# Kernel optimization log

Measured on AMD Instinct MI355X. Metric: run time of the kernel, lower is better.

The kernel has to match this reference:

```python
import jax, jax.numpy as jnp
import numpy as np
from jax import lax

VOCAB, ENC_DIM, PRED_H, JOINT_H = 4096, 1024, 640, 640
T, MAX_SYM, BLANK, SOS = 128, 30, 0, -1
S = T * (MAX_SYM + 1)  # upper bound on greedy-decode loop iterations


def setup_inputs() -> dict:
    key = jax.random.key(0)
    ks = jax.random.split(key, 10)
    rn = lambda k, shape, s: jax.random.normal(k, shape, jnp.float32) * s
    return {
        "enc_out": rn(ks[0], (1, T, ENC_DIM), 1.0),
        "out_len": T,
        "emb": rn(ks[1], (VOCAB, PRED_H), 0.1),
        "Wih0": rn(ks[2], (4 * PRED_H, PRED_H), 0.04),
        "Whh0": rn(ks[3], (4 * PRED_H, PRED_H), 0.04),
        "b0": jnp.zeros((4 * PRED_H,), jnp.float32),
        "Wih1": rn(ks[4], (4 * PRED_H, PRED_H), 0.04),
        "Whh1": rn(ks[5], (4 * PRED_H, PRED_H), 0.04),
        "b1": jnp.zeros((4 * PRED_H,), jnp.float32),
        "Wj1": rn(ks[6], (JOINT_H, ENC_DIM + PRED_H), 0.03),
        "bj1": jnp.zeros((JOINT_H,), jnp.float32),
        "Wj2": rn(ks[7], (VOCAB, JOINT_H), 0.04),
        "bj2": jnp.zeros((VOCAB,), jnp.float32),
    }


def _lstm_cell(x, h, c, Wih, Whh, b):
    z = x @ Wih.T + h @ Whh.T + b  # [4H], torch gate order i,f,g,o
    i, f, g, o = jnp.split(z, 4)
    c2 = jax.nn.sigmoid(f) * c + jax.nn.sigmoid(i) * jnp.tanh(g)
    return jax.nn.sigmoid(o) * jnp.tanh(c2), c2


def _decode(enc_out, timesteps, emb, Wih0, Whh0, b0, Wih1, Whh1, b1, Wj1, bj1, Wj2, bj2):
    enc = enc_out[0]  # [T, ENC_DIM]

    def step(carry, _):
        t, sa, last, h0, c0, h1, c1, labels, cnt, done = carry
        # prediction net step (SOS = -1 -> zero embedding)
        g_in = jnp.where(last < 0, 0.0, emb[jnp.maximum(last, 0)])
        h0n, c0n = _lstm_cell(g_in, h0, c0, Wih0, Whh0, b0)
        h1n, c1n = _lstm_cell(h0n, h1, c1, Wih1, Whh1, b1)
        # joint net on current encoder frame
        f = enc[jnp.minimum(t, T - 1)]
        hid = jax.nn.relu(Wj1 @ jnp.concatenate([f, h1n]) + bj1)
        logits = Wj2 @ hid + bj2  # [VOCAB]
        k = jnp.argmax(logits).astype(jnp.int32)
        stop_sym = (k == BLANK) | (sa >= MAX_SYM)
        emit = (~stop_sym) & (~done)
        adv = stop_sym & (~done)
        # emit: append symbol, keep hidden'; blank/max: advance time, discard hidden'
        last2 = jnp.where(emit, k, last)
        h0 = jnp.where(emit, h0n, h0); c0 = jnp.where(emit, c0n, c0)
        h1 = jnp.where(emit, h1n, h1); c1 = jnp.where(emit, c1n, c1)
        labels = labels.at[cnt].set(jnp.where(emit, k, labels[cnt]))
        cnt2 = cnt + emit.astype(jnp.int32)
        sa2 = jnp.where(emit, sa + 1, jnp.where(adv, 0, sa))
        t2 = t + adv.astype(jnp.int32)
        done2 = done | (adv & (t2 >= timesteps))
        out_logits = jnp.where(done, 0.0, logits)
        return (t2, sa2, last2, h0, c0, h1, c1, labels, cnt2, done2), out_logits

    zeros = jnp.zeros((PRED_H,), jnp.float32)
    carry0 = (jnp.int32(0), jnp.int32(0), jnp.int32(SOS),
              zeros, zeros, zeros, zeros,
              jnp.full((S,), -1, jnp.int32), jnp.int32(0), jnp.bool_(False))
    carry, logits_seq = lax.scan(step, carry0, None, length=S)
    labels, cnt = carry[7], carry[8]
    return logits_seq, labels, cnt


def reference(enc_out, out_len, emb, Wih0, Whh0, b0, Wih1, Whh1, b1, Wj1, bj1, Wj2, bj2):
    return _decode(enc_out, out_len, emb, Wih0, Whh0, b0, Wih1, Whh1, b1, Wj1, bj1, Wj2, bj2)
```

## Files before the change

kernel.cpp:

```cpp
#include <hip/hip_runtime.h>
#include <cmath>

#define VOCAB   4096
#define ENC_DIM 1024
#define PRED_H  640
#define JOINT_H 640
#define TMAX    128
#define MAX_SYM 30
#define NSTEPS  (TMAX*(MAX_SYM+1))
#define NWG     256
#define NTHR    512
#define RLX __ATOMIC_RELAXED
#define AGT __HIP_MEMORY_SCOPE_AGENT

typedef unsigned long long u64;


__device__ __forceinline__ float wave_red(float v){
  v += __shfl_xor(v, 32, 64);
  v += __shfl_xor(v, 16, 64);
  v += __shfl_xor(v,  8, 64);
  v += __shfl_xor(v,  4, 64);
  v += __shfl_xor(v,  2, 64);
  v += __shfl_xor(v,  1, 64);
  return v;
}

__device__ __forceinline__ float sigf(float x){ return 1.0f/(1.0f+expf(-x)); }

__device__ __forceinline__ void tstore(u64* p, float v, unsigned tag){
  __hip_atomic_store(p, ((u64)tag<<32) | (u64)__float_as_uint(v), RLX, AGT);
}
__device__ __forceinline__ float tpollv(u64* p, unsigned tag){
  u64 e = __hip_atomic_load(p, RLX, AGT);
  while ((unsigned)(e>>32) != tag){
    __builtin_amdgcn_s_sleep(4);
    e = __hip_atomic_load(p, RLX, AGT);
  }
  return __uint_as_float((unsigned)e);
}

__device__ __forceinline__ u64 mkentry(float lg, int r, unsigned ep){
  unsigned u = __float_as_uint(lg);
  u = (u & 0x80000000u) ? ~u : (u | 0x80000000u);
  return ((u64)u<<24) | ((u64)(ep&0xFFFu)<<12) | (u64)(4095 - r);
}

__global__ void init_ws(unsigned* ws){
  for (int i = threadIdx.x; i < 8192; i += 256) ws[i] = 0u;
}

__global__ __launch_bounds__(NTHR, 2)
void rnnt_decode(const float* __restrict__ enc,
                 const int*   __restrict__ outlen_p,
                 const float* __restrict__ emb,
                 const float* __restrict__ Wih0, const float* __restrict__ Whh0, const float* __restrict__ b0,
                 const float* __restrict__ Wih1, const float* __restrict__ Whh1, const float* __restrict__ b1,
                 const float* __restrict__ Wj1,  const float* __restrict__ bj1,
                 const float* __restrict__ Wj2,  const float* __restrict__ bj2,
                 float* __restrict__ out,
                 u64* __restrict__ parts,
                 u64* __restrict__ bufsT,
                 u64* __restrict__ hidT)
{
  const int wg = blockIdx.x, tid = threadIdx.x;
  const int wave = tid >> 6, lane = tid & 63;
  const int timesteps = outlen_p[0];

  __shared__ float xa[PRED_H];
  __shared__ float xsh[ENC_DIM];
  __shared__ float h0buf[2][PRED_H];
  __shared__ float h1buf[2][PRED_H];
  __shared__ float hidsh[JOINT_H];
  __shared__ float zsh[4][4];
  __shared__ float zjs[8];
  __shared__ float c0c[4], c1c[4], c0p[4], c1p[4];
  __shared__ u64 psh[8];
  __shared__ u64 pmx[4];

  const int jb = (wg*PRED_H)/NWG;
  const int je = ((wg+1)*PRED_H)/NWG;
  const int nj = je - jb;

  const int riA = wave, riB = wave + 8;
  const int gA = riA & 3, jA = riA >> 2;
  const int gB = riB & 3, jBx = riB >> 2;
  const bool hasB = (riB < 4*nj);
  const int rowA = gA*PRED_H + jb + jA;
  const int rowB = hasB ? (gB*PRED_H + jb + jBx) : 0;

  float w0xA[10], w0hA[10], w0xB[10], w0hB[10];
  float w1xA[10], w1hA[10], w1xB[10], w1hB[10];
  #pragma unroll
  for (int i = 0; i < 10; ++i){
    int c = lane + (i<<6);
    w0xA[i] = Wih0[(size_t)rowA*PRED_H + c];
    w0hA[i] = Whh0[(size_t)rowA*PRED_H + c];
    w1xA[i] = Wih1[(size_t)rowA*PRED_H + c];
    w1hA[i] = Whh1[(size_t)rowA*PRED_H + c];
    w0xB[i] = hasB ? Wih0[(size_t)rowB*PRED_H + c] : 0.f;
    w0hB[i] = hasB ? Whh0[(size_t)rowB*PRED_H + c] : 0.f;
    w1xB[i] = hasB ? Wih1[(size_t)rowB*PRED_H + c] : 0.f;
    w1hB[i] = hasB ? Whh1[(size_t)rowB*PRED_H + c] : 0.f;
  }
  const float bA0 = b0[rowA], bA1 = b1[rowA];
  const float bB0 = hasB ? b0[rowB] : 0.f, bB1 = hasB ? b1[rowB] : 0.f;

  const int vt = (wave < 4) ? wave*64 + lane : (wave-4)*64 + lane;
  float wjf0[4], wjh0[3], wjf2[4], wjh2[3];
  {
    int r0 = (wave < 4) ? jb : jb + 1;
    #pragma unroll
    for (int i = 0; i < 4; ++i) wjf0[i] = Wj1[(size_t)r0*(ENC_DIM+PRED_H) + vt + (i<<8)];
    #pragma unroll
    for (int i = 0; i < 3; ++i){
      int c = vt + (i<<8);
      wjh0[i] = (c < PRED_H) ? Wj1[(size_t)r0*(ENC_DIM+PRED_H) + ENC_DIM + c] : 0.f;
    }
    #pragma unroll
    for (int i = 0; i < 4; ++i) wjf2[i] = 0.f;
    #pragma unroll
    for (int i = 0; i < 3; ++i) wjh2[i] = 0.f;
    if (wave < 4 && nj == 3){
      int r2 = jb + 2;
      #pragma unroll
      for (int i = 0; i < 4; ++i) wjf2[i] = Wj1[(size_t)r2*(ENC_DIM+PRED_H) + vt + (i<<8)];
      #pragma unroll
      for (int i = 0; i < 3; ++i){
        int c = vt + (i<<8);
        wjh2[i] = (c < PRED_H) ? Wj1[(size_t)r2*(ENC_DIM+PRED_H) + ENC_DIM + c] : 0.f;
      }
    }
  }
  float bjr[3];
  bjr[0] = bj1[jb]; bjr[1] = bj1[jb+1]; bjr[2] = (nj == 3) ? bj1[jb+2] : 0.f;
  float ca0 = 0.f, ca2 = 0.f;

  const int rA2 = wg*16 + wave*2, rB2 = rA2 + 1;
  float wj2A[10], wj2B[10];
  #pragma unroll
  for (int i = 0; i < 10; ++i){
    int c = lane + (i<<6);
    wj2A[i] = Wj2[(size_t)rA2*JOINT_H + c];
    wj2B[i] = Wj2[(size_t)rB2*JOINT_H + c];
  }
  const float bjA2 = bj2[rA2], bjB2 = bj2[rB2];

  for (int i = tid; i < PRED_H; i += NTHR){ h0buf[0][i] = 0.f; h1buf[0][i] = 0.f; }
  if (tid < 4){ c0c[tid] = 0.f; c1c[tid] = 0.f; }
  __syncthreads();

  int cur = 0, t = 0, sa = 0, last = -1, cnt = 0, tStaged = -1;
  bool done = false, reuse = false;

  for (int s = 0; s < NSTEPS; ++s){
    if (done){
      if (wg < 8) out[(size_t)s*VOCAB + wg*NTHR + tid] = 0.f;
      continue;
    }
    const unsigned tag = (unsigned)(s + 1);

    if (!reuse){
      for (int i = tid; i < PRED_H; i += NTHR)
        xa[i] = (last >= 0) ? emb[(size_t)last*PRED_H + i] : 0.f;
      __syncthreads();
      {
        float acc = 0.f;
        #pragma unroll
        for (int i = 0; i < 10; ++i) acc = fmaf(w0xA[i], xa[lane+(i<<6)], acc);
        #pragma unroll
        for (int i = 0; i < 10; ++i) acc = fmaf(w0hA[i], h0buf[cur][lane+(i<<6)], acc);
        acc = wave_red(acc);
        if (lane == 0) zsh[gA][jA] = acc + bA0;
        if (hasB){
          float a2 = 0.f;
          #pragma unroll
          for (int i = 0; i < 10; ++i) a2 = fmaf(w0xB[i], xa[lane+(i<<6)], a2);
          #pragma unroll
          for (int i = 0; i < 10; ++i) a2 = fmaf(w0hB[i], h0buf[cur][lane+(i<<6)], a2);
          a2 = wave_red(a2);
          if (lane == 0) zsh[gB][jBx] = a2 + bB0;
        }
      }
      __syncthreads();
      if (tid < nj){
        float ig = sigf(zsh[0][tid]), fg = sigf(zsh[1][tid]);
        float gg = tanhf(zsh[2][tid]), og = sigf(zsh[3][tid]);
        float c2 = fg*c0c[tid] + ig*gg;
        c0p[tid] = c2;
        tstore(&bufsT[jb+tid], og*tanhf(c2), tag);
      }
      __syncthreads();

      for (int i = tid; i < PRED_H; i += NTHR)
        h0buf[cur^1][i] = tpollv(&bufsT[i], tag);
      __syncthreads();
      {
        float acc = 0.f;
        #pragma unroll
        for (int i = 0; i < 10; ++i) acc = fmaf(w1xA[i], h0buf[cur^1][lane+(i<<6)], acc);
        #pragma unroll
        for (int i = 0; i < 10; ++i) acc = fmaf(w1hA[i], h1buf[cur][lane+(i<<6)], acc);
        acc = wave_red(acc);
        if (lane == 0) zsh[gA][jA] = acc + bA1;
        if (hasB){
          float a2 = 0.f;
          #pragma unroll
          for (int i = 0; i < 10; ++i) a2 = fmaf(w1xB[i], h0buf[cur^1][lane+(i<<6)], a2);
          #pragma unroll
          for (int i = 0; i < 10; ++i) a2 = fmaf(w1hB[i], h1buf[cur][lane+(i<<6)], a2);
          a2 = wave_red(a2);
          if (lane == 0) zsh[gB][jBx] = a2 + bB1;
        }
      }
      __syncthreads();
      if (tid < nj){
        float ig = sigf(zsh[0][tid]), fg = sigf(zsh[1][tid]);
        float gg = tanhf(zsh[2][tid]), og = sigf(zsh[3][tid]);
        float c2 = fg*c1c[tid] + ig*gg;
        c1p[tid] = c2;
        tstore(&bufsT[PRED_H+jb+tid], og*tanhf(c2), tag);
      }
    }

    {
      int tcap = (t < TMAX-1) ? t : (TMAX-1);
      bool fNew = (tcap != tStaged);
      if (fNew)
        for (int i = tid; i < ENC_DIM; i += NTHR) xsh[i] = enc[(size_t)tcap*ENC_DIM + i];
      if (!reuse)
        for (int i = tid; i < PRED_H; i += NTHR)
          h1buf[cur^1][i] = tpollv(&bufsT[PRED_H+i], tag);
      __syncthreads();
      if (fNew){
        float a = 0.f;
        #pragma unroll
        for (int i = 0; i < 4; ++i) a = fmaf(wjf0[i], xsh[vt+(i<<8)], a);
        ca0 = a;
        if (wave < 4 && nj == 3){
          float a2 = 0.f;
          #pragma unroll
          for (int i = 0; i < 4; ++i) a2 = fmaf(wjf2[i], xsh[vt+(i<<8)], a2);
          ca2 = a2;
        }
        tStaged = tcap;
      }
      {
        float acc = ca0;
        #pragma unroll
        for (int i = 0; i < 3; ++i){
          int c = vt + (i<<8);
          acc = fmaf(wjh0[i], h1buf[cur^1][(c < PRED_H) ? c : 0], acc);
        }
        acc = wave_red(acc);
        if (lane == 0) zjs[wave] = acc;
      }
      __syncthreads();
      if (tid == 0){
        float v0 = zjs[0]+zjs[1]+zjs[2]+zjs[3] + bjr[0];
        tstore(&hidT[jb],   v0 > 0.f ? v0 : 0.f, tag);
        float v1 = zjs[4]+zjs[5]+zjs[6]+zjs[7] + bjr[1];
        tstore(&hidT[jb+1], v1 > 0.f ? v1 : 0.f, tag);
      }
      if (nj == 3){
        __syncthreads();
        if (wave < 4){
          float acc = ca2;
          #pragma unroll
          for (int i = 0; i < 3; ++i){
            int c = vt + (i<<8);
            acc = fmaf(wjh2[i], h1buf[cur^1][(c < PRED_H) ? c : 0], acc);
          }
          acc = wave_red(acc);
          if (lane == 0) zjs[wave] = acc;
        }
        __syncthreads();
        if (tid == 0){
          float v2 = zjs[0]+zjs[1]+zjs[2]+zjs[3] + bjr[2];
          tstore(&hidT[jb+2], v2 > 0.f ? v2 : 0.f, tag);
        }
      }
    }

    int k;
    {
      for (int i = tid; i < JOINT_H; i += NTHR)
        hidsh[i] = tpollv(&hidT[i], tag);
      __syncthreads();
      float accA = 0.f, accB = 0.f;
      #pragma unroll
      for (int i = 0; i < 10; ++i){
        float h = hidsh[lane+(i<<6)];
        accA = fmaf(wj2A[i], h, accA);
        accB = fmaf(wj2B[i], h, accB);
      }
      accA = wave_red(accA);
      accB = wave_red(accB);
      if (lane == 0){
        float lgA = accA + bjA2, lgB = accB + bjB2;
        out[(size_t)s*VOCAB + rA2] = lgA;
        out[(size_t)s*VOCAB + rB2] = lgB;
        u64 eA = mkentry(lgA, rA2, tag), eB = mkentry(lgB, rB2, tag);
        psh[wave] = eA > eB ? eA : eB;
      }
      __syncthreads();
      if (tid == 0){
        u64 m = psh[0];
        #pragma unroll
        for (int w = 1; w < 8; ++w) if (psh[w] > m) m = psh[w];
        __hip_atomic_store(&parts[wg], m, RLX, AGT);
      }
      u64 myp = 0;
      if (tid < 256){
        u64 e = __hip_atomic_load(&parts[tid], RLX, AGT);
        while ((unsigned)((e>>12) & 0xFFFu) != (tag & 0xFFFu)){
          __builtin_amdgcn_s_sleep(2);
          e = __hip_atomic_load(&parts[tid], RLX, AGT);
        }
        myp = e;
      }
      if (wave < 4){
        #pragma unroll
        for (int off = 32; off; off >>= 1){
          u64 o = __shfl_xor(myp, off, 64);
          if (o > myp) myp = o;
        }
        if (lane == 0) pmx[wave] = myp;
      }
      __syncthreads();
      u64 m = pmx[0];
      if (pmx[1] > m) m = pmx[1];
      if (pmx[2] > m) m = pmx[2];
      if (pmx[3] > m) m = pmx[3];
      k = 4095 - (int)(m & 0xFFFull);
    }

    bool stop = (k == 0) || (sa >= MAX_SYM);
    if (!stop){
      if (wg == 0 && tid == 0) out[(size_t)NSTEPS*VOCAB + cnt] = (float)k;
      if (tid < nj){ c0c[tid] = c0p[tid]; c1c[tid] = c1p[tid]; }
      cnt++; sa++; last = k; cur ^= 1; reuse = false;
    } else {
      sa = 0; t++; reuse = true;
      if (t >= timesteps) done = true;
    }
    __syncthreads();
  }

  size_t lab = (size_t)NSTEPS*VOCAB;
  int gidx = wg*NTHR + tid;
  for (int i = cnt + gidx; i < NSTEPS; i += NWG*NTHR) out[lab + i] = -1.f;
  if (wg == 0 && tid == 0) out[lab + NSTEPS] = (float)cnt;
}

extern "C" void kernel_launch(void* const* d_in, const int* in_sizes, int n_in,
                              void* d_out, int out_size, void* d_ws, size_t ws_size,
                              hipStream_t stream) {
  const float* enc  = (const float*)d_in[0];
  const int*   olen = (const int*)  d_in[1];
  const float* emb  = (const float*)d_in[2];
  const float* Wih0 = (const float*)d_in[3];
  const float* Whh0 = (const float*)d_in[4];
  const float* b0   = (const float*)d_in[5];
  const float* Wih1 = (const float*)d_in[6];
  const float* Whh1 = (const float*)d_in[7];
  const float* b1   = (const float*)d_in[8];
  const float* Wj1  = (const float*)d_in[9];
  const float* bj1  = (const float*)d_in[10];
  const float* Wj2  = (const float*)d_in[11];
  const float* bj2  = (const float*)d_in[12];
  float* out = (float*)d_out;

  u64* parts = (u64*)d_ws;
  u64* bufsT = (u64*)((char*)d_ws + 4096);
  u64* hidT  = (u64*)((char*)d_ws + 16384);

  init_ws<<<1, 256, 0, stream>>>((unsigned*)d_ws);

  void* args[] = {&enc,&olen,&emb,&Wih0,&Whh0,&b0,&Wih1,&Whh1,&b1,
                  &Wj1,&bj1,&Wj2,&bj2,&out,&parts,&bufsT,&hidT};
  hipLaunchCooperativeKernel((const void*)rnnt_decode, dim3(NWG), dim3(NTHR),
                             args, 0, stream);
}
```

Baseline: 51.19 ms.

## Replace tagged per-element polling with counter barriers and vector cache-bypass loads

Swaps the per-element tagged 64-bit stores and polls for plain float stores plus a per-phase atomic arrival counter. One thread per workgroup spins on the counter, then 160 threads fetch the shared vector with dwordx4 loads that bypass the cache. The argmax partials drop the epoch tag and use the same counter, and the third joint-hidden row is computed alongside the first two, which removes extra syncthreads. The aim is fewer global atomics and polls on each step of the serial decode, at the cost of relying on release ordering through waitcnt before the relaxed counter increment.

```diff
diff --git a/kernel.cpp b/kernel.cpp
--- a/kernel.cpp
+++ b/kernel.cpp
@@ -14,6 +14,8 @@
 #define AGT __HIP_MEMORY_SCOPE_AGENT
 
 typedef unsigned long long u64;
+typedef __attribute__((ext_vector_type(4))) float f32x4;
+typedef __attribute__((ext_vector_type(4))) unsigned int u32x4;
 
 
 __device__ __forceinline__ float wave_red(float v){
@@ -28,22 +30,28 @@
 
 __device__ __forceinline__ float sigf(float x){ return 1.0f/(1.0f+expf(-x)); }
 
-__device__ __forceinline__ void tstore(u64* p, float v, unsigned tag){
-  __hip_atomic_store(p, ((u64)tag<<32) | (u64)__float_as_uint(v), RLX, AGT);
-}
-__device__ __forceinline__ float tpollv(u64* p, unsigned tag){
-  u64 e = __hip_atomic_load(p, RLX, AGT);
-  while ((unsigned)(e>>32) != tag){
-    __builtin_amdgcn_s_sleep(4);
-    e = __hip_atomic_load(p, RLX, AGT);
-  }
-  return __uint_as_float((unsigned)e);
-}
-
-__device__ __forceinline__ u64 mkentry(float lg, int r, unsigned ep){
+__device__ __forceinline__ void cstore_f(float* p, float v){
+  __hip_atomic_store((unsigned*)p, __float_as_uint(v), RLX, AGT);
+}
+__device__ __forceinline__ void cstore_u64(u64* p, u64 v){
+  __hip_atomic_store(p, v, RLX, AGT);
+}
+
+__device__ __forceinline__ f32x4 cload_f4(const float* p){
+  f32x4 r;
+  asm volatile("global_load_dwordx4 %0, %1, off sc0 sc1" : "=v"(r) : "v"(p));
+  return r;
+}
+__device__ __forceinline__ u32x4 cload_u4(const u64* p){
+  u32x4 r;
+  asm volatile("global_load_dwordx4 %0, %1, off sc0 sc1" : "=v"(r) : "v"(p));
+  return r;
+}
+
+__device__ __forceinline__ u64 mkentry(float lg, int r){
   unsigned u = __float_as_uint(lg);
   u = (u & 0x80000000u) ? ~u : (u | 0x80000000u);
-  return ((u64)u<<24) | ((u64)(ep&0xFFFu)<<12) | (u64)(4095 - r);
+  return ((u64)u<<32) | (u64)(4095 - r);
 }
 
 __global__ void init_ws(unsigned* ws){
@@ -59,13 +67,17 @@
                  const float* __restrict__ Wj1,  const float* __restrict__ bj1,
                  const float* __restrict__ Wj2,  const float* __restrict__ bj2,
                  float* __restrict__ out,
+                 unsigned* __restrict__ cnts,
                  u64* __restrict__ parts,
-                 u64* __restrict__ bufsT,
-                 u64* __restrict__ hidT)
+                 float* __restrict__ h0n,
+                 float* __restrict__ h1n,
+                 float* __restrict__ hidg)
 {
   const int wg = blockIdx.x, tid = threadIdx.x;
   const int wave = tid >> 6, lane = tid & 63;
   const int timesteps = outlen_p[0];
+  unsigned* cntA = cnts;      unsigned* cntB = cnts + 16;
+  unsigned* cntH = cnts + 32; unsigned* cntP = cnts + 48;
 
   __shared__ float xa[PRED_H];
   __shared__ float xsh[ENC_DIM];
@@ -74,9 +86,11 @@
   __shared__ float hidsh[JOINT_H];
   __shared__ float zsh[4][4];
   __shared__ float zjs[8];
+  __shared__ float zjs2[4];
   __shared__ float c0c[4], c1c[4], c0p[4], c1p[4];
   __shared__ u64 psh[8];
-  __shared__ u64 pmx[4];
+  __shared__ u64 pm[128];
+  __shared__ int kshm;
 
   const int jb = (wg*PRED_H)/NWG;
   const int je = ((wg+1)*PRED_H)/NWG;
@@ -151,6 +165,7 @@
   __syncthreads();
 
   int cur = 0, t = 0, sa = 0, last = -1, cnt = 0, tStaged = -1;
+  unsigned eA = 0, eB = 0, eH = 0, eP = 0;
   bool done = false, reuse = false;
 
   for (int s = 0; s < NSTEPS; ++s){
@@ -158,9 +173,9 @@
       if (wg < 8) out[(size_t)s*VOCAB + wg*NTHR + tid] = 0.f;
       continue;
     }
-    const unsigned tag = (unsigned)(s + 1);
 
     if (!reuse){
+      ++eA; ++eB;
       for (int i = tid; i < PRED_H; i += NTHR)
         xa[i] = (last >= 0) ? emb[(size_t)last*PRED_H + i] : 0.f;
       __syncthreads();
@@ -188,12 +203,22 @@
         float gg = tanhf(zsh[2][tid]), og = sigf(zsh[3][tid]);
         float c2 = fg*c0c[tid] + ig*gg;
         c0p[tid] = c2;
-        tstore(&bufsT[jb+tid], og*tanhf(c2), tag);
-      }
-      __syncthreads();
-
-      for (int i = tid; i < PRED_H; i += NTHR)
-        h0buf[cur^1][i] = tpollv(&bufsT[i], tag);
+        cstore_f(&h0n[jb+tid], og*tanhf(c2));
+      }
+      asm volatile("s_waitcnt vmcnt(0)" ::: "memory");
+      if (tid == 0) __hip_atomic_fetch_add(cntA, 1u, RLX, AGT);
+
+      if (tid == 0){
+        while (__hip_atomic_load(cntA, RLX, AGT) < eA*NWG) __builtin_amdgcn_s_sleep(1);
+      }
+      __syncthreads();
+      {
+        f32x4 v;
+        if (tid < 160) v = cload_f4(h0n + (tid<<2));
+        asm volatile("s_waitcnt vmcnt(0)" ::: "memory");
+        __builtin_amdgcn_sched_barrier(0);
+        if (tid < 160) *(f32x4*)&h0buf[cur^1][tid<<2] = v;
+      }
       __syncthreads();
       {
         float acc = 0.f;
@@ -219,18 +244,29 @@
         float gg = tanhf(zsh[2][tid]), og = sigf(zsh[3][tid]);
         float c2 = fg*c1c[tid] + ig*gg;
         c1p[tid] = c2;
-        tstore(&bufsT[PRED_H+jb+tid], og*tanhf(c2), tag);
-      }
+        cstore_f(&h1n[jb+tid], og*tanhf(c2));
+      }
+      asm volatile("s_waitcnt vmcnt(0)" ::: "memory");
+      if (tid == 0) __hip_atomic_fetch_add(cntB, 1u, RLX, AGT);
     }
 
     {
+      ++eH;
       int tcap = (t < TMAX-1) ? t : (TMAX-1);
       bool fNew = (tcap != tStaged);
       if (fNew)
         for (int i = tid; i < ENC_DIM; i += NTHR) xsh[i] = enc[(size_t)tcap*ENC_DIM + i];
-      if (!reuse)
-        for (int i = tid; i < PRED_H; i += NTHR)
-          h1buf[cur^1][i] = tpollv(&bufsT[PRED_H+i], tag);
+      if (!reuse){
+        if (tid == 0){
+          while (__hip_atomic_load(cntB, RLX, AGT) < eB*NWG) __builtin_amdgcn_s_sleep(1);
+        }
+        __syncthreads();
+        f32x4 v;
+        if (tid < 160) v = cload_f4(h1n + (tid<<2));
+        asm volatile("s_waitcnt vmcnt(0)" ::: "memory");
+        __builtin_amdgcn_sched_barrier(0);
+        if (tid < 160) *(f32x4*)&h1buf[cur^1][tid<<2] = v;
+      }
       __syncthreads();
       if (fNew){
         float a = 0.f;
@@ -255,37 +291,45 @@
         acc = wave_red(acc);
         if (lane == 0) zjs[wave] = acc;
       }
+      if (wave < 4 && nj == 3){
+        float acc = ca2;
+        #pragma unroll
+        for (int i = 0; i < 3; ++i){
+          int c = vt + (i<<8);
+          acc = fmaf(wjh2[i], h1buf[cur^1][(c < PRED_H) ? c : 0], acc);
+        }
+        acc = wave_red(acc);
+        if (lane == 0) zjs2[wave] = acc;
+      }
       __syncthreads();
       if (tid == 0){
         float v0 = zjs[0]+zjs[1]+zjs[2]+zjs[3] + bjr[0];
-        tstore(&hidT[jb],   v0 > 0.f ? v0 : 0.f, tag);
+        cstore_f(&hidg[jb],   v0 > 0.f ? v0 : 0.f);
         float v1 = zjs[4]+zjs[5]+zjs[6]+zjs[7] + bjr[1];
-        tstore(&hidT[jb+1], v1 > 0.f ? v1 : 0.f, tag);
-      }
-      if (nj == 3){
-        __syncthreads();
-        if (wave < 4){
-          float acc = ca2;
-          #pragma unroll
-          for (int i = 0; i < 3; ++i){
-            int c = vt + (i<<8);
-            acc = fmaf(wjh2[i], h1buf[cur^1][(c < PRED_H) ? c : 0], acc);
-          }
-          acc = wave_red(acc);
-          if (lane == 0) zjs[wave] = acc;
-        }
-        __syncthreads();
-        if (tid == 0){
-          float v2 = zjs[0]+zjs[1]+zjs[2]+zjs[3] + bjr[2];
-          tstore(&hidT[jb+2], v2 > 0.f ? v2 : 0.f, tag);
-        }
+        cstore_f(&hidg[jb+1], v1 > 0.f ? v1 : 0.f);
+        if (nj == 3){
+          float v2 = zjs2[0]+zjs2[1]+zjs2[2]+zjs2[3] + bjr[2];
+          cstore_f(&hidg[jb+2], v2 > 0.f ? v2 : 0.f);
+        }
+        asm volatile("s_waitcnt vmcnt(0)" ::: "memory");
+        __hip_atomic_fetch_add(cntH, 1u, RLX, AGT);
       }
     }
 
     int k;
     {
-      for (int i = tid; i < JOINT_H; i += NTHR)
-        hidsh[i] = tpollv(&hidT[i], tag);
+      ++eP;
+      if (tid == 0){
+        while (__hip_atomic_load(cntH, RLX, AGT) < eH*NWG) __builtin_amdgcn_s_sleep(1);
+      }
+      __syncthreads();
+      {
+        f32x4 v;
+        if (tid < 160) v = cload_f4(hidg + (tid<<2));
+        asm volatile("s_waitcnt vmcnt(0)" ::: "memory");
+        __builtin_amdgcn_sched_barrier(0);
+        if (tid < 160) *(f32x4*)&hidsh[tid<<2] = v;
+      }
       __syncthreads();
       float accA = 0.f, accB = 0.f;
       #pragma unroll
@@ -300,39 +344,43 @@
         float lgA = accA + bjA2, lgB = accB + bjB2;
         out[(size_t)s*VOCAB + rA2] = lgA;
         out[(size_t)s*VOCAB + rB2] = lgB;
-        u64 eA = mkentry(lgA, rA2, tag), eB = mkentry(lgB, rB2, tag);
-        psh[wave] = eA > eB ? eA : eB;
+        u64 eAe = mkentry(lgA, rA2), eBe = mkentry(lgB, rB2);
+        psh[wave] = eAe > eBe ? eAe : eBe;
       }
       __syncthreads();
       if (tid == 0){
         u64 m = psh[0];
         #pragma unroll
         for (int w = 1; w < 8; ++w) if (psh[w] > m) m = psh[w];
-        __hip_atomic_store(&parts[wg], m, RLX, AGT);
-      }
-      u64 myp = 0;
-      if (tid < 256){
-        u64 e = __hip_atomic_load(&parts[tid], RLX, AGT);
-        while ((unsigned)((e>>12) & 0xFFFu) != (tag & 0xFFFu)){
-          __builtin_amdgcn_s_sleep(2);
-          e = __hip_atomic_load(&parts[tid], RLX, AGT);
-        }
-        myp = e;
-      }
-      if (wave < 4){
+        cstore_u64(&parts[wg], m);
+        asm volatile("s_waitcnt vmcnt(0)" ::: "memory");
+        __hip_atomic_fetch_add(cntP, 1u, RLX, AGT);
+        while (__hip_atomic_load(cntP, RLX, AGT) < eP*NWG) __builtin_amdgcn_s_sleep(1);
+      }
+      __syncthreads();
+      {
+        u32x4 pv;
+        if (tid < 128) pv = cload_u4(&parts[tid<<1]);
+        asm volatile("s_waitcnt vmcnt(0)" ::: "memory");
+        __builtin_amdgcn_sched_barrier(0);
+        if (tid < 128){
+          u64 e0 = ((u64)pv.y<<32) | pv.x;
+          u64 e1 = ((u64)pv.w<<32) | pv.z;
+          pm[tid] = e0 > e1 ? e0 : e1;
+        }
+      }
+      __syncthreads();
+      if (wave == 0){
+        u64 m = pm[lane] > pm[lane+64] ? pm[lane] : pm[lane+64];
         #pragma unroll
         for (int off = 32; off; off >>= 1){
-          u64 o = __shfl_xor(myp, off, 64);
-          if (o > myp) myp = o;
-        }
-        if (lane == 0) pmx[wave] = myp;
-      }
-      __syncthreads();
-      u64 m = pmx[0];
-      if (pmx[1] > m) m = pmx[1];
-      if (pmx[2] > m) m = pmx[2];
-      if (pmx[3] > m) m = pmx[3];
-      k = 4095 - (int)(m & 0xFFFull);
+          u64 o = __shfl_xor(m, off, 64);
+          if (o > m) m = o;
+        }
+        if (lane == 0) kshm = 4095 - (int)(m & 0xFFFull);
+      }
+      __syncthreads();
+      k = kshm;
     }
 
     bool stop = (k == 0) || (sa >= MAX_SYM);
@@ -371,14 +419,16 @@
   const float* bj2  = (const float*)d_in[12];
   float* out = (float*)d_out;
 
-  u64* parts = (u64*)d_ws;
-  u64* bufsT = (u64*)((char*)d_ws + 4096);
-  u64* hidT  = (u64*)((char*)d_ws + 16384);
+  unsigned* cnts = (unsigned*)d_ws;
+  u64* parts = (u64*)((char*)d_ws + 256);
+  float* h0n = (float*)((char*)d_ws + 2560);
+  float* h1n = (float*)((char*)d_ws + 5120);
+  float* hidg = (float*)((char*)d_ws + 7680);
 
   init_ws<<<1, 256, 0, stream>>>((unsigned*)d_ws);
 
   void* args[] = {&enc,&olen,&emb,&Wih0,&Whh0,&b0,&Wih1,&Whh1,&b1,
-                  &Wj1,&bj1,&Wj2,&bj2,&out,&parts,&bufsT,&hidT};
+                  &Wj1,&bj1,&Wj2,&bj2,&out,&cnts,&parts,&h0n,&h1n,&hidg};
   hipLaunchCooperativeKernel((const void*)rnnt_decode, dim3(NWG), dim3(NTHR),
                              args, 0, stream);
 }
```

New measurement: 84.98 ms. 1.66x slower.
